# Optimization experiments

Measured on AMD Instinct MI355X. Metric: run time of the kernel, lower is better.

The kernel has to match this reference:

```python
import jax, jax.numpy as jnp
import numpy as np

E, H, I = 5, 768, 1024  # num_experts, hidden_dim, intermediate_dim
TOP_K = 2


def setup_inputs() -> dict:
    key = jax.random.key(0)
    ks = jax.random.split(key, 6)
    s = 0.02
    return {
        "x": jax.random.normal(ks[0], (4, 2048, H), dtype=jnp.float32),
        "router_w": jax.random.normal(ks[1], (E, H), dtype=jnp.float32) * s,  # torch Linear (out,in)
        "router_b": jnp.zeros((E,), dtype=jnp.float32),
        "gate_w": jax.random.normal(ks[2], (E, H, I), dtype=jnp.float32) * s,
        "up_w": jax.random.normal(ks[3], (E, H, I), dtype=jnp.float32) * s,
        "down_w": jax.random.normal(ks[4], (E, I, H), dtype=jnp.float32) * s,
    }


def reference(x, router_w, router_b, gate_w, up_w, down_w):
    B, S, Hd = x.shape
    xf = x.reshape(-1, Hd)                       # [T, H]
    T = xf.shape[0]
    # Router: linear (with bias) -> softmax -> top-2 -> renormalize
    logits = xf @ router_w.T + router_b          # [T, E]
    scores = jax.nn.softmax(logits, axis=-1)
    vals, idx = jax.lax.top_k(scores, TOP_K)     # [T, 2]
    vals = vals / jnp.sum(vals, axis=-1, keepdims=True)
    # Dense combine weights: zero for unselected experts (same math as the
    # per-expert gather/scatter loop in the original module).
    comb = jnp.zeros((T, gate_w.shape[0]), dtype=x.dtype)
    comb = comb.at[jnp.arange(T)[:, None], idx].add(vals)  # [T, E]
    # SwiGLU per expert, vectorized over experts
    g = jnp.einsum('th,ehi->tei', xf, gate_w)    # [T, E, I]
    u = jnp.einsum('th,ehi->tei', xf, up_w)
    y = jnp.einsum('tei,eih->teh', jax.nn.silu(g) * u, down_w)  # [T, E, H]
    out = jnp.einsum('teh,te->th', y, comb)
    return out.reshape(B, S, Hd)
```

## Files before the change

### kernel.cpp

```cpp
#include <hip/hip_runtime.h>
#include <hip/hip_bf16.h>
#include <cstdint>
#include <cstddef>

#define T_TOK 8192
#define H_DIM 768
#define I_DIM 1024
#define N_EXP 5
#define MAXTILE 136

typedef short v8s __attribute__((ext_vector_type(8)));
typedef float v4f __attribute__((ext_vector_type(4)));

static __device__ __forceinline__ unsigned short f2bf(float f) {
    union { float f; unsigned int u; } v; v.f = f;
    unsigned int u = v.u;
    unsigned int r = (u + 0x7fffu + ((u >> 16) & 1u)) >> 16;
    return (unsigned short)r;
}
static __device__ __forceinline__ float bf2f(unsigned short s) {
    union { unsigned int u; float f; } v; v.u = ((unsigned int)s) << 16; return v.f;
}

static __device__ __forceinline__ void async16(const unsigned short* g, unsigned short* l) {
    __builtin_amdgcn_global_load_lds(
        (const __attribute__((address_space(1))) unsigned int*)g,
        (__attribute__((address_space(3))) unsigned int*)l, 16, 0, 0);
}

__global__ void k_transp_all(const float* __restrict__ gw, const float* __restrict__ uw,
                             const float* __restrict__ dw,
                             unsigned short* __restrict__ wbt, unsigned short* __restrict__ dbt) {
    __shared__ float tile[32][33];
    const int z = blockIdx.z;
    const int tid = threadIdx.x;
    const int row = tid >> 3, cq = tid & 7;
    const int ocol = tid >> 3, seg = tid & 7;
    if (z < 2 * N_EXP) {
        if (blockIdx.y >= H_DIM / 32) return;
        const int e = z % N_EXP;
        const int isUp = z >= N_EXP;
        const float* src = (isUp ? uw : gw) + (size_t)e * H_DIM * I_DIM;
        const int c0 = blockIdx.x * 32, r0 = blockIdx.y * 32;
        float4 v = *(const float4*)(src + (size_t)(r0 + row) * I_DIM + c0 + cq * 4);
        tile[row][cq * 4 + 0] = v.x; tile[row][cq * 4 + 1] = v.y;
        tile[row][cq * 4 + 2] = v.z; tile[row][cq * 4 + 3] = v.w;
        __syncthreads();
        int c = c0 + ocol;
        int orow = (c >> 4) * 32 + (c & 15) + (isUp ? 16 : 0);
        ushort4 o;
        o.x = f2bf(tile[seg * 4 + 0][ocol]); o.y = f2bf(tile[seg * 4 + 1][ocol]);
        o.z = f2bf(tile[seg * 4 + 2][ocol]); o.w = f2bf(tile[seg * 4 + 3][ocol]);
        *(ushort4*)(wbt + ((size_t)e * 2 * I_DIM + orow) * H_DIM + r0 + seg * 4) = o;
    } else {
        if (blockIdx.x >= H_DIM / 32) return;
        const int e = z - 2 * N_EXP;
        const float* src = dw + (size_t)e * I_DIM * H_DIM;
        unsigned short* dst = dbt + (size_t)e * I_DIM * H_DIM;
        const int c0 = blockIdx.x * 32, r0 = blockIdx.y * 32;
        float4 v = *(const float4*)(src + (size_t)(r0 + row) * H_DIM + c0 + cq * 4);
        tile[row][cq * 4 + 0] = v.x; tile[row][cq * 4 + 1] = v.y;
        tile[row][cq * 4 + 2] = v.z; tile[row][cq * 4 + 3] = v.w;
        __syncthreads();
        ushort4 o;
        o.x = f2bf(tile[seg * 4 + 0][ocol]); o.y = f2bf(tile[seg * 4 + 1][ocol]);
        o.z = f2bf(tile[seg * 4 + 2][ocol]); o.w = f2bf(tile[seg * 4 + 3][ocol]);
        *(ushort4*)(dst + (size_t)(c0 + ocol) * I_DIM + r0 + seg * 4) = o;
    }
}

__global__ void k_router_a(const float* __restrict__ x, const float* __restrict__ rw,
                           const float* __restrict__ rb,
                           unsigned short* __restrict__ xb,
                           int* __restrict__ top2e, float2* __restrict__ top2w) {
    const int wave = threadIdx.x >> 6, lane = threadIdx.x & 63;
    const int t = blockIdx.x * 4 + wave;
    const float* xr = x + (size_t)t * H_DIM;
    unsigned short* xbr = xb + (size_t)t * H_DIM;
    float acc[N_EXP];
#pragma unroll
    for (int e = 0; e < N_EXP; e++) acc[e] = 0.f;
#pragma unroll
    for (int j = 0; j < H_DIM / 256; j++) {
        int idx = j * 256 + lane * 4;
        float4 xv = *(const float4*)(xr + idx);
        ushort4 o;
        o.x = f2bf(xv.x); o.y = f2bf(xv.y); o.z = f2bf(xv.z); o.w = f2bf(xv.w);
        *(ushort4*)(xbr + idx) = o;
#pragma unroll
        for (int e = 0; e < N_EXP; e++) {
            float4 wv = *(const float4*)(rw + e * H_DIM + idx);
            acc[e] += xv.x * wv.x + xv.y * wv.y + xv.z * wv.z + xv.w * wv.w;
        }
    }
#pragma unroll
    for (int s = 32; s > 0; s >>= 1) {
#pragma unroll
        for (int e = 0; e < N_EXP; e++) acc[e] += __shfl_down(acc[e], s);
    }
    if (lane == 0) {
        float l[N_EXP];
#pragma unroll
        for (int e = 0; e < N_EXP; e++) l[e] = acc[e] + rb[e];
        int i1 = 0;
#pragma unroll
        for (int e = 1; e < N_EXP; e++) if (l[e] > l[i1]) i1 = e;
        int i2 = (i1 == 0) ? 1 : 0;
#pragma unroll
        for (int e = 0; e < N_EXP; e++) if (e != i1 && l[e] > l[i2]) i2 = e;
        float w1 = 1.f / (1.f + __expf(l[i2] - l[i1]));
        top2e[t] = i1 | (i2 << 8);
        top2w[t] = make_float2(w1, 1.f - w1);
    }
}

__global__ void k_router_b(const int* __restrict__ top2e, const float2* __restrict__ top2w,
                           int* __restrict__ cnt, int* __restrict__ tokslot,
                           float* __restrict__ pweight, int* __restrict__ done,
                           int4* __restrict__ tiles) {
    __shared__ int lcnt[N_EXP], lbase[N_EXP];
    const int tid = threadIdx.x;
    if (tid < N_EXP) lcnt[tid] = 0;
    __syncthreads();
    const int t = blockIdx.x * 256 + tid;
    const int pe = top2e[t];
    const float2 wv = top2w[t];
    const int e1 = pe & 0xff, e2 = pe >> 8;
    const int s1 = atomicAdd(&lcnt[e1], 1);
    const int s2 = atomicAdd(&lcnt[e2], 1);
    __syncthreads();
    if (tid < N_EXP) lbase[tid] = atomicAdd(&cnt[tid], lcnt[tid]);
    __syncthreads();
    const int p1 = lbase[e1] + s1;
    tokslot[e1 * T_TOK + p1] = t; pweight[e1 * T_TOK + p1] = wv.x;
    const int p2 = lbase[e2] + s2;
    tokslot[e2 * T_TOK + p2] = t | (1 << 16); pweight[e2 * T_TOK + p2] = wv.y;
    __syncthreads();
    if (tid == 0) {
        __threadfence();
        if (atomicAdd(done, 1) == (int)gridDim.x - 1) {
            int c[N_EXP], off = 0, idx = 0;
            for (int e = 0; e < N_EXP; e++) c[e] = atomicAdd(&cnt[e], 0);
            for (int e = 0; e < N_EXP; e++) {
                for (int m0 = 0; m0 < c[e]; m0 += 128)
                    tiles[idx++] = make_int4(e, m0, off, c[e]);
                off += c[e];
            }
            for (; idx < MAXTILE; idx++) tiles[idx] = make_int4(-1, 0, 0, 0);
        }
    }
}

__launch_bounds__(256, 4)
__global__ void k_gateup(const unsigned short* __restrict__ xb,
                         const unsigned short* __restrict__ wbt,
                         const int4* __restrict__ tiles,
                         const int* __restrict__ tokslot,
                         const float* __restrict__ pweight,
                         unsigned short* __restrict__ hbuf) {
    const int4 td = tiles[blockIdx.x];
    const int e = td.x;
    if (e < 0) return;
    const int m0 = td.y, offe = td.z, cn = td.w;
    const int n0 = blockIdx.y * 64;

    __shared__ __align__(16) unsigned short ldsA[2][128 * 32];
    __shared__ __align__(16) unsigned short ldsB[2][128 * 32];
    __shared__ int tokLds[128];
    __shared__ float pwLds[128];

    const int tid = threadIdx.x;
    if (tid < 128) {
        int gr = m0 + tid;
        int tk = 0; float pw = 0.f;
        if (gr < cn) { tk = tokslot[e * T_TOK + gr] & 0xFFFF; pw = pweight[e * T_TOK + gr]; }
        tokLds[tid] = tk; pwLds[tid] = pw;
    }
    __syncthreads();

    const int lane = tid & 63;
    const int wave = tid >> 6;
    const int fm = lane & 15, quad = lane >> 4;

    const int srow = wave * 16 + (lane >> 2);
    const int scol = (lane & 3) * 8;
    const unsigned short* aG1 = xb + (size_t)tokLds[srow] * H_DIM + scol;
    const unsigned short* aG2 = xb + (size_t)tokLds[64 + srow] * H_DIM + scol;
    const unsigned short* bG1 = wbt + ((size_t)e * 2 * I_DIM + n0 * 2 + srow) * H_DIM + scol;
    const unsigned short* bG2 = bG1 + (size_t)64 * H_DIM;
    const int ldsOff = wave * 512;

    const int wm = (wave & 1) * 64, wnw = wave >> 1;

    v4f acc[4][4];
#pragma unroll
    for (int i = 0; i < 4; i++)
#pragma unroll
        for (int j = 0; j < 4; j++) acc[i][j] = (v4f)0.f;

    {
        async16(aG1, &ldsA[0][ldsOff]);
        async16(aG2, &ldsA[0][2048 + ldsOff]);
        async16(bG1, &ldsB[0][ldsOff]);
        async16(bG2, &ldsB[0][2048 + ldsOff]);
    }
    const int NIT = H_DIM / 32;
    for (int kb = 0; kb < NIT; kb++) {
        const int cur = kb & 1;
        __syncthreads();
        if (kb + 1 < NIT) {
            const int k0 = (kb + 1) * 32;
            async16(aG1 + k0, &ldsA[1 - cur][ldsOff]);
            async16(aG2 + k0, &ldsA[1 - cur][2048 + ldsOff]);
            async16(bG1 + k0, &ldsB[1 - cur][ldsOff]);
            async16(bG2 + k0, &ldsB[1 - cur][2048 + ldsOff]);
        }
        v8s aF[4], bF[4];
#pragma unroll
        for (int im = 0; im < 4; im++)
            aF[im] = *(const v8s*)&ldsA[cur][(wm + im * 16 + fm) * 32 + quad * 8];
#pragma unroll
        for (int in = 0; in < 4; in++)
            bF[in] = *(const v8s*)&ldsB[cur][(wnw * 64 + in * 16 + fm) * 32 + quad * 8];
#pragma unroll
        for (int im = 0; im < 4; im++)
#pragma unroll
            for (int in = 0; in < 4; in++)
                acc[im][in] = __builtin_amdgcn_mfma_f32_16x16x32_bf16(aF[im], bF[in], acc[im][in], 0, 0, 0);
    }

#pragma unroll
    for (int im = 0; im < 4; im++) {
#pragma unroll
        for (int reg = 0; reg < 4; reg++) {
            int lr = wm + im * 16 + quad * 4 + reg;
            int gr = m0 + lr;
            if (gr < cn) {
                float pw = pwLds[lr];
                size_t base = (size_t)(offe + gr) * I_DIM + n0 + wnw * 32 + fm;
#pragma unroll
                for (int j = 0; j < 2; j++) {
                    float g = acc[im][2 * j][reg];
                    float u = acc[im][2 * j + 1][reg];
                    float s = g / (1.f + __expf(-g));
                    hbuf[base + j * 16] = f2bf(s * u * pw);
                }
            }
        }
    }
}

__launch_bounds__(256, 4)
__global__ void k_down(const unsigned short* __restrict__ hbuf,
                       const unsigned short* __restrict__ dbt,
                       const int4* __restrict__ tiles,
                       const int* __restrict__ tokslot,
                       unsigned short* __restrict__ ybuf) {
    const int4 td = tiles[blockIdx.x];
    const int e = td.x;
    if (e < 0) return;
    const int m0 = td.y, offe = td.z, cn = td.w;
    const int n0 = blockIdx.y * 128;

    __shared__ __align__(16) unsigned short ldsA[2][128 * 32];
    __shared__ __align__(16) unsigned short ldsB[2][128 * 32];
    __shared__ int tokLds[128];

    const int tid = threadIdx.x;
    if (tid < 128) {
        int gr = m0 + tid;
        tokLds[tid] = (gr < cn) ? tokslot[e * T_TOK + gr] : 0;
    }
    __syncthreads();

    const int lane = tid & 63;
    const int wave = tid >> 6;
    const int fm = lane & 15, quad = lane >> 4;

    const int srow = wave * 16 + (lane >> 2);
    const int scol = (lane & 3) * 8;
    int ar1 = m0 + srow;      if (ar1 >= cn) ar1 = cn - 1;
    int ar2 = m0 + 64 + srow; if (ar2 >= cn) ar2 = cn - 1;
    const unsigned short* aG1 = hbuf + (size_t)(offe + ar1) * I_DIM + scol;
    const unsigned short* aG2 = hbuf + (size_t)(offe + ar2) * I_DIM + scol;
    const unsigned short* bG1 = dbt + ((size_t)e * H_DIM + n0 + srow) * I_DIM + scol;
    const unsigned short* bG2 = bG1 + (size_t)64 * I_DIM;
    const int ldsOff = wave * 512;

    const int wm = (wave & 1) * 64, wn = (wave >> 1) * 64;

    v4f acc[4][4];
#pragma unroll
    for (int i = 0; i < 4; i++)
#pragma unroll
        for (int j = 0; j < 4; j++) acc[i][j] = (v4f)0.f;

    {
        async16(aG1, &ldsA[0][ldsOff]);
        async16(aG2, &ldsA[0][2048 + ldsOff]);
        async16(bG1, &ldsB[0][ldsOff]);
        async16(bG2, &ldsB[0][2048 + ldsOff]);
    }
    const int NIT = I_DIM / 32;
    for (int kb = 0; kb < NIT; kb++) {
        const int cur = kb & 1;
        __syncthreads();
        if (kb + 1 < NIT) {
            const int k0 = (kb + 1) * 32;
            async16(aG1 + k0, &ldsA[1 - cur][ldsOff]);
            async16(aG2 + k0, &ldsA[1 - cur][2048 + ldsOff]);
            async16(bG1 + k0, &ldsB[1 - cur][ldsOff]);
            async16(bG2 + k0, &ldsB[1 - cur][2048 + ldsOff]);
        }
        v8s aF[4], bF[4];
#pragma unroll
        for (int im = 0; im < 4; im++)
            aF[im] = *(const v8s*)&ldsA[cur][(wm + im * 16 + fm) * 32 + quad * 8];
#pragma unroll
        for (int in = 0; in < 4; in++)
            bF[in] = *(const v8s*)&ldsB[cur][(wn + in * 16 + fm) * 32 + quad * 8];
#pragma unroll
        for (int im = 0; im < 4; im++)
#pragma unroll
            for (int in = 0; in < 4; in++)
                acc[im][in] = __builtin_amdgcn_mfma_f32_16x16x32_bf16(aF[im], bF[in], acc[im][in], 0, 0, 0);
    }

#pragma unroll
    for (int im = 0; im < 4; im++) {
#pragma unroll
        for (int reg = 0; reg < 4; reg++) {
            int lr = wm + im * 16 + quad * 4 + reg;
            int gr = m0 + lr;
            if (gr < cn) {
                int v = tokLds[lr];
                int tok = v & 0xFFFF, s = (v >> 16) & 1;
#pragma unroll
                for (int in = 0; in < 4; in++) {
                    int col = n0 + wn + in * 16 + fm;
                    ybuf[((size_t)s * T_TOK + tok) * H_DIM + col] = f2bf(acc[im][in][reg]);
                }
            }
        }
    }
}

__global__ void k_combine(const unsigned short* __restrict__ ybuf, float* __restrict__ out) {
    const size_t i8 = ((size_t)blockIdx.x * 256 + threadIdx.x) * 8;
    const unsigned short* y0 = ybuf + i8;
    const unsigned short* y1 = ybuf + (size_t)T_TOK * H_DIM + i8;
    ushort4 a0 = *(const ushort4*)y0, a1 = *(const ushort4*)(y0 + 4);
    ushort4 b0 = *(const ushort4*)y1, b1 = *(const ushort4*)(y1 + 4);
    float4 o0, o1;
    o0.x = bf2f(a0.x) + bf2f(b0.x); o0.y = bf2f(a0.y) + bf2f(b0.y);
    o0.z = bf2f(a0.z) + bf2f(b0.z); o0.w = bf2f(a0.w) + bf2f(b0.w);
    o1.x = bf2f(a1.x) + bf2f(b1.x); o1.y = bf2f(a1.y) + bf2f(b1.y);
    o1.z = bf2f(a1.z) + bf2f(b1.z); o1.w = bf2f(a1.w) + bf2f(b1.w);
    *(float4*)(out + i8) = o0;
    *(float4*)(out + i8 + 4) = o1;
}

extern "C" void kernel_launch(void* const* d_in, const int* in_sizes, int n_in,
                              void* d_out, int out_size, void* d_ws, size_t ws_size,
                              hipStream_t stream) {
    const float* x  = (const float*)d_in[0];
    const float* rw = (const float*)d_in[1];
    const float* rb = (const float*)d_in[2];
    const float* gw = (const float*)d_in[3];
    const float* uw = (const float*)d_in[4];
    const float* dw = (const float*)d_in[5];
    float* out = (float*)d_out;

    char* ws = (char*)d_ws;
    size_t o = 0;
    auto alloc = [&](size_t bytes) { void* p = ws + o; o += (bytes + 255) & ~255ull; return p; };
    int*    cnt     = (int*)   alloc(8 * 4);
    int*    tokslot = (int*)   alloc((size_t)N_EXP * T_TOK * 4);
    float*  pweight = (float*) alloc((size_t)N_EXP * T_TOK * 4);
    int*    top2e   = (int*)   alloc((size_t)T_TOK * 4);
    float2* top2w   = (float2*)alloc((size_t)T_TOK * 8);
    int4*   tiles   = (int4*)  alloc((size_t)MAXTILE * 16);
    unsigned short* xb   = (unsigned short*)alloc((size_t)T_TOK * H_DIM * 2);
    unsigned short* wbt  = (unsigned short*)alloc((size_t)N_EXP * 2 * I_DIM * H_DIM * 2);
    unsigned short* dbt  = (unsigned short*)alloc((size_t)N_EXP * H_DIM * I_DIM * 2);
    unsigned short* hbuf = (unsigned short*)alloc((size_t)(2 * T_TOK + 128) * I_DIM * 2);
    unsigned short* ybuf = (unsigned short*)alloc((size_t)2 * T_TOK * H_DIM * 2);

    hipMemsetAsync(cnt, 0, 8 * 4, stream);

    dim3 tg(I_DIM / 32, I_DIM / 32, 3 * N_EXP);
    k_transp_all<<<tg, 256, 0, stream>>>(gw, uw, dw, wbt, dbt);

    k_router_a<<<T_TOK / 4, 256, 0, stream>>>(x, rw, rb, xb, top2e, top2w);
    k_router_b<<<T_TOK / 256, 256, 0, stream>>>(top2e, top2w, cnt, tokslot, pweight,
                                                cnt + 5, tiles);

    dim3 g1(MAXTILE, I_DIM / 64);
    k_gateup<<<g1, 256, 0, stream>>>(xb, wbt, tiles, tokslot, pweight, hbuf);

    dim3 g2(MAXTILE, H_DIM / 128);
    k_down<<<g2, 256, 0, stream>>>(hbuf, dbt, tiles, tokslot, ybuf);

    k_combine<<<(T_TOK * H_DIM) / (256 * 8), 256, 0, stream>>>(ybuf, out);
}
```

Measured before the change: 265.5 us.

## Triple-buffer GEMM LDS pipeline and merge weight transpose with router kernel

Both grouped GEMM kernels move from double to triple buffering of LDS tiles. Each iteration now uses a partial vmcnt wait plus a raw barrier, so two stages of global-to-LDS loads stay in flight instead of draining all loads at every __syncthreads. Occupancy hints drop from 4 to 3 blocks because LDS use grows. Separately, the weight transpose/convert kernel and the router kernel are merged into one launch using extra z-slices, which removes a launch boundary and lets the two run concurrently.

```diff
diff --git a/kernel.cpp b/kernel.cpp
--- a/kernel.cpp
+++ b/kernel.cpp
@@ -28,89 +28,91 @@
         (__attribute__((address_space(3))) unsigned int*)l, 16, 0, 0);
 }
 
-__global__ void k_transp_all(const float* __restrict__ gw, const float* __restrict__ uw,
-                             const float* __restrict__ dw,
-                             unsigned short* __restrict__ wbt, unsigned short* __restrict__ dbt) {
-    __shared__ float tile[32][33];
+#define WAIT_VM4() __builtin_amdgcn_s_waitcnt(0x0F74)
+
+__global__ void k_prep(const float* __restrict__ gw, const float* __restrict__ uw,
+                       const float* __restrict__ dw,
+                       unsigned short* __restrict__ wbt, unsigned short* __restrict__ dbt,
+                       const float* __restrict__ x, const float* __restrict__ rw,
+                       const float* __restrict__ rb, unsigned short* __restrict__ xb,
+                       int* __restrict__ top2e, float2* __restrict__ top2w) {
     const int z = blockIdx.z;
     const int tid = threadIdx.x;
-    const int row = tid >> 3, cq = tid & 7;
-    const int ocol = tid >> 3, seg = tid & 7;
-    if (z < 2 * N_EXP) {
-        if (blockIdx.y >= H_DIM / 32) return;
-        const int e = z % N_EXP;
-        const int isUp = z >= N_EXP;
-        const float* src = (isUp ? uw : gw) + (size_t)e * H_DIM * I_DIM;
-        const int c0 = blockIdx.x * 32, r0 = blockIdx.y * 32;
-        float4 v = *(const float4*)(src + (size_t)(r0 + row) * I_DIM + c0 + cq * 4);
-        tile[row][cq * 4 + 0] = v.x; tile[row][cq * 4 + 1] = v.y;
-        tile[row][cq * 4 + 2] = v.z; tile[row][cq * 4 + 3] = v.w;
-        __syncthreads();
-        int c = c0 + ocol;
-        int orow = (c >> 4) * 32 + (c & 15) + (isUp ? 16 : 0);
-        ushort4 o;
-        o.x = f2bf(tile[seg * 4 + 0][ocol]); o.y = f2bf(tile[seg * 4 + 1][ocol]);
-        o.z = f2bf(tile[seg * 4 + 2][ocol]); o.w = f2bf(tile[seg * 4 + 3][ocol]);
-        *(ushort4*)(wbt + ((size_t)e * 2 * I_DIM + orow) * H_DIM + r0 + seg * 4) = o;
+    if (z < 3 * N_EXP) {
+        __shared__ float tile[32][33];
+        const int row = tid >> 3, cq = tid & 7;
+        const int ocol = tid >> 3, seg = tid & 7;
+        if (z < 2 * N_EXP) {
+            if (blockIdx.y >= H_DIM / 32) return;
+            const int e = z % N_EXP;
+            const int isUp = z >= N_EXP;
+            const float* src = (isUp ? uw : gw) + (size_t)e * H_DIM * I_DIM;
+            const int c0 = blockIdx.x * 32, r0 = blockIdx.y * 32;
+            float4 v = *(const float4*)(src + (size_t)(r0 + row) * I_DIM + c0 + cq * 4);
+            tile[row][cq * 4 + 0] = v.x; tile[row][cq * 4 + 1] = v.y;
+            tile[row][cq * 4 + 2] = v.z; tile[row][cq * 4 + 3] = v.w;
+            __syncthreads();
+            int c = c0 + ocol;
+            int orow = (c >> 4) * 32 + (c & 15) + (isUp ? 16 : 0);
+            ushort4 o;
+            o.x = f2bf(tile[seg * 4 + 0][ocol]); o.y = f2bf(tile[seg * 4 + 1][ocol]);
+            o.z = f2bf(tile[seg * 4 + 2][ocol]); o.w = f2bf(tile[seg * 4 + 3][ocol]);
+            *(ushort4*)(wbt + ((size_t)e * 2 * I_DIM + orow) * H_DIM + r0 + seg * 4) = o;
+        } else {
+            if (blockIdx.x >= H_DIM / 32) return;
+            const int e = z - 2 * N_EXP;
+            const float* src = dw + (size_t)e * I_DIM * H_DIM;
+            unsigned short* dst = dbt + (size_t)e * I_DIM * H_DIM;
+            const int c0 = blockIdx.x * 32, r0 = blockIdx.y * 32;
+            float4 v = *(const float4*)(src + (size_t)(r0 + row) * H_DIM + c0 + cq * 4);
+            tile[row][cq * 4 + 0] = v.x; tile[row][cq * 4 + 1] = v.y;
+            tile[row][cq * 4 + 2] = v.z; tile[row][cq * 4 + 3] = v.w;
+            __syncthreads();
+            ushort4 o;
+            o.x = f2bf(tile[seg * 4 + 0][ocol]); o.y = f2bf(tile[seg * 4 + 1][ocol]);
+            o.z = f2bf(tile[seg * 4 + 2][ocol]); o.w = f2bf(tile[seg * 4 + 3][ocol]);
+            *(ushort4*)(dst + (size_t)(c0 + ocol) * I_DIM + r0 + seg * 4) = o;
+        }
     } else {
-        if (blockIdx.x >= H_DIM / 32) return;
-        const int e = z - 2 * N_EXP;
-        const float* src = dw + (size_t)e * I_DIM * H_DIM;
-        unsigned short* dst = dbt + (size_t)e * I_DIM * H_DIM;
-        const int c0 = blockIdx.x * 32, r0 = blockIdx.y * 32;
-        float4 v = *(const float4*)(src + (size_t)(r0 + row) * H_DIM + c0 + cq * 4);
-        tile[row][cq * 4 + 0] = v.x; tile[row][cq * 4 + 1] = v.y;
-        tile[row][cq * 4 + 2] = v.z; tile[row][cq * 4 + 3] = v.w;
-        __syncthreads();
-        ushort4 o;
-        o.x = f2bf(tile[seg * 4 + 0][ocol]); o.y = f2bf(tile[seg * 4 + 1][ocol]);
-        o.z = f2bf(tile[seg * 4 + 2][ocol]); o.w = f2bf(tile[seg * 4 + 3][ocol]);
-        *(ushort4*)(dst + (size_t)(c0 + ocol) * I_DIM + r0 + seg * 4) = o;
-    }
-}
-
-__global__ void k_router_a(const float* __restrict__ x, const float* __restrict__ rw,
-                           const float* __restrict__ rb,
-                           unsigned short* __restrict__ xb,
-                           int* __restrict__ top2e, float2* __restrict__ top2w) {
-    const int wave = threadIdx.x >> 6, lane = threadIdx.x & 63;
-    const int t = blockIdx.x * 4 + wave;
-    const float* xr = x + (size_t)t * H_DIM;
-    unsigned short* xbr = xb + (size_t)t * H_DIM;
-    float acc[N_EXP];
-#pragma unroll
-    for (int e = 0; e < N_EXP; e++) acc[e] = 0.f;
-#pragma unroll
-    for (int j = 0; j < H_DIM / 256; j++) {
-        int idx = j * 256 + lane * 4;
-        float4 xv = *(const float4*)(xr + idx);
-        ushort4 o;
-        o.x = f2bf(xv.x); o.y = f2bf(xv.y); o.z = f2bf(xv.z); o.w = f2bf(xv.w);
-        *(ushort4*)(xbr + idx) = o;
-#pragma unroll
-        for (int e = 0; e < N_EXP; e++) {
-            float4 wv = *(const float4*)(rw + e * H_DIM + idx);
-            acc[e] += xv.x * wv.x + xv.y * wv.y + xv.z * wv.z + xv.w * wv.w;
-        }
-    }
-#pragma unroll
-    for (int s = 32; s > 0; s >>= 1) {
-#pragma unroll
-        for (int e = 0; e < N_EXP; e++) acc[e] += __shfl_down(acc[e], s);
-    }
-    if (lane == 0) {
-        float l[N_EXP];
-#pragma unroll
-        for (int e = 0; e < N_EXP; e++) l[e] = acc[e] + rb[e];
-        int i1 = 0;
-#pragma unroll
-        for (int e = 1; e < N_EXP; e++) if (l[e] > l[i1]) i1 = e;
-        int i2 = (i1 == 0) ? 1 : 0;
-#pragma unroll
-        for (int e = 0; e < N_EXP; e++) if (e != i1 && l[e] > l[i2]) i2 = e;
-        float w1 = 1.f / (1.f + __expf(l[i2] - l[i1]));
-        top2e[t] = i1 | (i2 << 8);
-        top2w[t] = make_float2(w1, 1.f - w1);
+        const int wave = tid >> 6, lane = tid & 63;
+        const int t = (((z - 3 * N_EXP) * 1024 + blockIdx.y * 32 + blockIdx.x) * 4) + wave;
+        const float* xr = x + (size_t)t * H_DIM;
+        unsigned short* xbr = xb + (size_t)t * H_DIM;
+        float acc[N_EXP];
+#pragma unroll
+        for (int e = 0; e < N_EXP; e++) acc[e] = 0.f;
+#pragma unroll
+        for (int j = 0; j < H_DIM / 256; j++) {
+            int idx = j * 256 + lane * 4;
+            float4 xv = *(const float4*)(xr + idx);
+            ushort4 o;
+            o.x = f2bf(xv.x); o.y = f2bf(xv.y); o.z = f2bf(xv.z); o.w = f2bf(xv.w);
+            *(ushort4*)(xbr + idx) = o;
+#pragma unroll
+            for (int e = 0; e < N_EXP; e++) {
+                float4 wv = *(const float4*)(rw + e * H_DIM + idx);
+                acc[e] += xv.x * wv.x + xv.y * wv.y + xv.z * wv.z + xv.w * wv.w;
+            }
+        }
+#pragma unroll
+        for (int s = 32; s > 0; s >>= 1) {
+#pragma unroll
+            for (int e = 0; e < N_EXP; e++) acc[e] += __shfl_down(acc[e], s);
+        }
+        if (lane == 0) {
+            float l[N_EXP];
+#pragma unroll
+            for (int e = 0; e < N_EXP; e++) l[e] = acc[e] + rb[e];
+            int i1 = 0;
+#pragma unroll
+            for (int e = 1; e < N_EXP; e++) if (l[e] > l[i1]) i1 = e;
+            int i2 = (i1 == 0) ? 1 : 0;
+#pragma unroll
+            for (int e = 0; e < N_EXP; e++) if (e != i1 && l[e] > l[i2]) i2 = e;
+            float w1 = 1.f / (1.f + __expf(l[i2] - l[i1]));
+            top2e[t] = i1 | (i2 << 8);
+            top2w[t] = make_float2(w1, 1.f - w1);
+        }
     }
 }
 
@@ -151,7 +153,7 @@
     }
 }
 
-__launch_bounds__(256, 4)
+__launch_bounds__(256, 3)
 __global__ void k_gateup(const unsigned short* __restrict__ xb,
                          const unsigned short* __restrict__ wbt,
                          const int4* __restrict__ tiles,
@@ -164,8 +166,8 @@
     const int m0 = td.y, offe = td.z, cn = td.w;
     const int n0 = blockIdx.y * 64;
 
-    __shared__ __align__(16) unsigned short ldsA[2][128 * 32];
-    __shared__ __align__(16) unsigned short ldsB[2][128 * 32];
+    __shared__ __align__(16) unsigned short ldsA[3][128 * 32];
+    __shared__ __align__(16) unsigned short ldsB[3][128 * 32];
     __shared__ int tokLds[128];
     __shared__ float pwLds[128];
 
@@ -198,22 +200,27 @@
 #pragma unroll
         for (int j = 0; j < 4; j++) acc[i][j] = (v4f)0.f;
 
-    {
-        async16(aG1, &ldsA[0][ldsOff]);
-        async16(aG2, &ldsA[0][2048 + ldsOff]);
-        async16(bG1, &ldsB[0][ldsOff]);
-        async16(bG2, &ldsB[0][2048 + ldsOff]);
-    }
     const int NIT = H_DIM / 32;
+    async16(aG1, &ldsA[0][ldsOff]);
+    async16(aG2, &ldsA[0][2048 + ldsOff]);
+    async16(bG1, &ldsB[0][ldsOff]);
+    async16(bG2, &ldsB[0][2048 + ldsOff]);
+    async16(aG1 + 32, &ldsA[1][ldsOff]);
+    async16(aG2 + 32, &ldsA[1][2048 + ldsOff]);
+    async16(bG1 + 32, &ldsB[1][ldsOff]);
+    async16(bG2 + 32, &ldsB[1][2048 + ldsOff]);
+
     for (int kb = 0; kb < NIT; kb++) {
-        const int cur = kb & 1;
-        __syncthreads();
-        if (kb + 1 < NIT) {
-            const int k0 = (kb + 1) * 32;
-            async16(aG1 + k0, &ldsA[1 - cur][ldsOff]);
-            async16(aG2 + k0, &ldsA[1 - cur][2048 + ldsOff]);
-            async16(bG1 + k0, &ldsB[1 - cur][ldsOff]);
-            async16(bG2 + k0, &ldsB[1 - cur][2048 + ldsOff]);
+        const int cur = kb % 3;
+        WAIT_VM4();
+        __builtin_amdgcn_s_barrier();
+        {
+            const int kpf = (kb + 2 < NIT ? kb + 2 : NIT - 1) * 32;
+            const int nb = (kb + 2) % 3;
+            async16(aG1 + kpf, &ldsA[nb][ldsOff]);
+            async16(aG2 + kpf, &ldsA[nb][2048 + ldsOff]);
+            async16(bG1 + kpf, &ldsB[nb][ldsOff]);
+            async16(bG2 + kpf, &ldsB[nb][2048 + ldsOff]);
         }
         v8s aF[4], bF[4];
 #pragma unroll
@@ -250,7 +257,7 @@
     }
 }
 
-__launch_bounds__(256, 4)
+__launch_bounds__(256, 3)
 __global__ void k_down(const unsigned short* __restrict__ hbuf,
                        const unsigned short* __restrict__ dbt,
                        const int4* __restrict__ tiles,
@@ -262,8 +269,8 @@
     const int m0 = td.y, offe = td.z, cn = td.w;
     const int n0 = blockIdx.y * 128;
 
-    __shared__ __align__(16) unsigned short ldsA[2][128 * 32];
-    __shared__ __align__(16) unsigned short ldsB[2][128 * 32];
+    __shared__ __align__(16) unsigned short ldsA[3][128 * 32];
+    __shared__ __align__(16) unsigned short ldsB[3][128 * 32];
     __shared__ int tokLds[128];
 
     const int tid = threadIdx.x;
@@ -295,22 +302,27 @@
 #pragma unroll
         for (int j = 0; j < 4; j++) acc[i][j] = (v4f)0.f;
 
-    {
-        async16(aG1, &ldsA[0][ldsOff]);
-        async16(aG2, &ldsA[0][2048 + ldsOff]);
-        async16(bG1, &ldsB[0][ldsOff]);
-        async16(bG2, &ldsB[0][2048 + ldsOff]);
-    }
     const int NIT = I_DIM / 32;
+    async16(aG1, &ldsA[0][ldsOff]);
+    async16(aG2, &ldsA[0][2048 + ldsOff]);
+    async16(bG1, &ldsB[0][ldsOff]);
+    async16(bG2, &ldsB[0][2048 + ldsOff]);
+    async16(aG1 + 32, &ldsA[1][ldsOff]);
+    async16(aG2 + 32, &ldsA[1][2048 + ldsOff]);
+    async16(bG1 + 32, &ldsB[1][ldsOff]);
+    async16(bG2 + 32, &ldsB[1][2048 + ldsOff]);
+
     for (int kb = 0; kb < NIT; kb++) {
-        const int cur = kb & 1;
-        __syncthreads();
-        if (kb + 1 < NIT) {
-            const int k0 = (kb + 1) * 32;
-            async16(aG1 + k0, &ldsA[1 - cur][ldsOff]);
-            async16(aG2 + k0, &ldsA[1 - cur][2048 + ldsOff]);
-            async16(bG1 + k0, &ldsB[1 - cur][ldsOff]);
-            async16(bG2 + k0, &ldsB[1 - cur][2048 + ldsOff]);
+        const int cur = kb % 3;
+        WAIT_VM4();
+        __builtin_amdgcn_s_barrier();
+        {
+            const int kpf = (kb + 2 < NIT ? kb + 2 : NIT - 1) * 32;
+            const int nb = (kb + 2) % 3;
+            async16(aG1 + kpf, &ldsA[nb][ldsOff]);
+            async16(aG2 + kpf, &ldsA[nb][2048 + ldsOff]);
+            async16(bG1 + kpf, &ldsB[nb][ldsOff]);
+            async16(bG2 + kpf, &ldsB[nb][2048 + ldsOff]);
         }
         v8s aF[4], bF[4];
 #pragma unroll
@@ -388,10 +400,9 @@
 
     hipMemsetAsync(cnt, 0, 8 * 4, stream);
 
-    dim3 tg(I_DIM / 32, I_DIM / 32, 3 * N_EXP);
-    k_transp_all<<<tg, 256, 0, stream>>>(gw, uw, dw, wbt, dbt);
-
-    k_router_a<<<T_TOK / 4, 256, 0, stream>>>(x, rw, rb, xb, top2e, top2w);
+    dim3 pg(I_DIM / 32, I_DIM / 32, 3 * N_EXP + 2);
+    k_prep<<<pg, 256, 0, stream>>>(gw, uw, dw, wbt, dbt, x, rw, rb, xb, top2e, top2w);
+
     k_router_b<<<T_TOK / 256, 256, 0, stream>>>(top2e, top2w, cnt, tokslot, pweight,
                                                 cnt + 5, tiles);
 
```

After: 268.9 us. No clear change (+1.3%).
